# Performance work log

Measured on AMD Instinct MI355X. Metric: run time of the kernel, lower is better.

The kernel has to match this reference:

```python
import jax, jax.numpy as jnp
import numpy as np

N = 4096
IN_F = 128
OUT_F = 64
H = 4
NEG_SLOPE = 0.2


def setup_inputs() -> dict:
    key = jax.random.key(0)
    kx, ka, kw, kadj = jax.random.split(key, 4)
    x = jax.random.normal(kx, (N, IN_F), dtype=jnp.float32)
    adj = (jax.random.uniform(kadj, (N, N)) < 0.01).astype(jnp.float32)
    # xavier-uniform-ish params
    W = jax.random.uniform(kw, (IN_F, OUT_F * H), dtype=jnp.float32,
                           minval=-1.0, maxval=1.0) * float(np.sqrt(6.0 / (IN_F + OUT_F * H)))
    a = jax.random.uniform(ka, (H, 2 * OUT_F), dtype=jnp.float32,
                           minval=-1.0, maxval=1.0) * float(np.sqrt(6.0 / (H + 2 * OUT_F)))
    return {"x": x, "adj": adj, "W": W, "a": a}


def reference(x, adj, W, a):
    n = x.shape[0]
    h = (x @ W).reshape(n, H, OUT_F)                      # [N,H,F]
    a_src = a[:, :OUT_F]                                  # [H,F]
    a_tgt = a[:, OUT_F:]                                  # [H,F]
    attn_src = jnp.einsum('nhf,hf->nh', h, a_src)         # [N,H]
    attn_tgt = jnp.einsum('nhf,hf->nh', h, a_tgt)         # [N,H]
    # e[i,h,j] = attn_src[i,h] + attn_tgt[j,h]
    e = attn_src[:, :, None] + attn_tgt.T[None, :, :]     # [N,H,N]
    e = jnp.where(e > 0, e, NEG_SLOPE * e)                # leaky_relu(0.2)
    adj_self = adj + jnp.eye(n, dtype=adj.dtype)
    mask = (adj_self != 0)[:, None, :]                    # [N,1,N]
    e = jnp.where(mask, e, -jnp.inf)
    attention = jax.nn.softmax(e, axis=-1)                # [N,H,N]
    attention = jnp.nan_to_num(attention, nan=0.0)
    # dropout is identity at eval time
    out = jnp.einsum('nhj,jhf->nhf', attention, h)        # [N,H,F]
    return out.reshape(n, H * OUT_F)
```

## Files before the change

kernel.cpp:

```cpp
#include <hip/hip_runtime.h>
#include <hip/hip_bf16.h>

#define N_NODES 4096
#define IN_FEAT 128
#define OUT_FEAT 64
#define NHEAD 4
#define HID 256
#define NEG_SLOPE 0.2f
#define MAXC 256
#define GEMM_BLOCKS 256
#define SCAN_BLOCKS 1024

typedef float f4 __attribute__((ext_vector_type(4)));

__global__ __launch_bounds__(256) void k_prep(
    const float* __restrict__ x, const float* __restrict__ adj,
    const float* __restrict__ W, const float* __restrict__ a,
    float* __restrict__ h, float* __restrict__ attn_src,
    float* __restrict__ attn_tgt,
    unsigned short* __restrict__ nbrs, int* __restrict__ deg)
{
    __shared__ f4 xs4[64][32];
    __shared__ float red_s[4][64];
    __shared__ float red_t[4][64];

    const int t = threadIdx.x;
    const int lane = t & 63;
    const int wv = t >> 6;

    if (blockIdx.x < GEMM_BLOCKS) {
        const int rb = blockIdx.x >> 2;
        const int cb = blockIdx.x & 3;
        const int row0 = rb * 64;
        const int tc4 = (t >> 4) * 4;
        const int c0 = cb * 64 + tc4;
        const int tr = t & 15;

        {
            const f4* xg = reinterpret_cast<const f4*>(x) + (size_t)row0 * 32;
            const int kq = t & 31;
            #pragma unroll
            for (int it = 0; it < 8; ++it) {
                const int r = it * 8 + (t >> 5);
                xs4[r][kq ^ ((r >> 2) & 7)] = xg[r * 32 + kq];
            }
        }
        __syncthreads();

        f4 acc[4] = {};

        for (int kq = 0; kq < 32; ++kq) {
            f4 wvv[4];
            #pragma unroll
            for (int kk = 0; kk < 4; ++kk)
                wvv[kk] = *reinterpret_cast<const f4*>(W + (kq * 4 + kk) * HID + c0);
            f4 xv[4];
            #pragma unroll
            for (int j = 0; j < 4; ++j)
                xv[j] = xs4[tr * 4 + j][kq ^ (tr & 7)];
            #pragma unroll
            for (int kk = 0; kk < 4; ++kk)
                #pragma unroll
                for (int j = 0; j < 4; ++j)
                    acc[j] += xv[j][kk] * wvv[kk];
        }

        #pragma unroll
        for (int j = 0; j < 4; ++j) {
            const int row = row0 + tr * 4 + j;
            *reinterpret_cast<f4*>(h + (size_t)row * HID + c0) = acc[j];
        }

        const f4 asv = *reinterpret_cast<const f4*>(a + cb * 2 * OUT_FEAT + tc4);
        const f4 atv = *reinterpret_cast<const f4*>(a + cb * 2 * OUT_FEAT + OUT_FEAT + tc4);
        #pragma unroll
        for (int j = 0; j < 4; ++j) {
            float s = acc[j][0] * asv[0] + acc[j][1] * asv[1]
                    + acc[j][2] * asv[2] + acc[j][3] * asv[3];
            float g = acc[j][0] * atv[0] + acc[j][1] * atv[1]
                    + acc[j][2] * atv[2] + acc[j][3] * atv[3];
            s += __shfl_xor(s, 16, 64); s += __shfl_xor(s, 32, 64);
            g += __shfl_xor(g, 16, 64); g += __shfl_xor(g, 32, 64);
            if (((t >> 4) & 3) == 0) {
                red_s[wv][tr * 4 + j] = s;
                red_t[wv][tr * 4 + j] = g;
            }
        }
        __syncthreads();
        if (t < 64) {
            const float s = red_s[0][t] + red_s[1][t] + red_s[2][t] + red_s[3][t];
            const float g = red_t[0][t] + red_t[1][t] + red_t[2][t] + red_t[3][t];
            attn_src[(row0 + t) * NHEAD + cb] = s;
            attn_tgt[(row0 + t) * NHEAD + cb] = g;
        }
    } else {
        const int i = (blockIdx.x - GEMM_BLOCKS) * 4 + wv;

        const float4* arow = reinterpret_cast<const float4*>(adj + (size_t)i * N_NODES);
        float4 v[16];
        #pragma unroll
        for (int u = 0; u < 16; ++u) v[u] = arow[u * 64 + lane];

        unsigned long long m = 0ull;
        #pragma unroll
        for (int u = 0; u < 16; ++u) {
            const int jb = u * 256 + lane * 4;
            if (v[u].x != 0.f || (jb + 0) == i) m |= 1ull << (u * 4 + 0);
            if (v[u].y != 0.f || (jb + 1) == i) m |= 1ull << (u * 4 + 1);
            if (v[u].z != 0.f || (jb + 2) == i) m |= 1ull << (u * 4 + 2);
            if (v[u].w != 0.f || (jb + 3) == i) m |= 1ull << (u * 4 + 3);
        }
        const int cnt = __popcll(m);

        int incl = cnt;
        #pragma unroll
        for (int d = 1; d < 64; d <<= 1) {
            int u2 = __shfl_up(incl, d, 64);
            if (lane >= d) incl += u2;
        }
        int off = incl - cnt;
        if (lane == 63) deg[i] = (incl < MAXC) ? incl : MAXC;

        unsigned short* nl = nbrs + (size_t)i * MAXC;
        unsigned long long mm = m;
        while (mm) {
            const int b = __ffsll((unsigned long long)mm) - 1;
            mm &= mm - 1;
            const int j = ((b >> 2) * 256) + lane * 4 + (b & 3);
            if (off < MAXC) nl[off] = (unsigned short)j;
            ++off;
        }
    }
}

__global__ __launch_bounds__(256) void k_agg(
    const unsigned short* __restrict__ nbrs, const int* __restrict__ deg,
    const float* __restrict__ h, const float* __restrict__ attn_src,
    const float* __restrict__ attn_tgt, float* __restrict__ out)
{
    __shared__ float p[NHEAD][MAXC];
    __shared__ unsigned short nl[MAXC];

    const int i = blockIdx.x;
    const int t = threadIdx.x;
    const int lane = t & 63;
    const int head = t >> 6;

    const int d = deg[i];
    nl[t] = (t < d) ? nbrs[(size_t)i * MAXC + t] : (unsigned short)0;
    __syncthreads();

    const float srcv = attn_src[i * NHEAD + head];
    const int rnd = (d + 3) & ~3;
    float lmax = -1e30f;
    for (int idx = lane; idx < rnd; idx += 64) {
        if (idx < d) {
            float e = srcv + attn_tgt[nl[idx] * NHEAD + head];
            e = (e > 0.f) ? e : NEG_SLOPE * e;
            p[head][idx] = e;
            lmax = fmaxf(lmax, e);
        } else {
            p[head][idx] = 0.f;
        }
    }
    #pragma unroll
    for (int s = 32; s; s >>= 1) lmax = fmaxf(lmax, __shfl_xor(lmax, s, 64));
    float ssum = 0.f;
    for (int idx = lane; idx < d; idx += 64) {
        float pe = __expf(p[head][idx] - lmax);
        p[head][idx] = pe;
        ssum += pe;
    }
    #pragma unroll
    for (int s = 32; s; s >>= 1) ssum += __shfl_xor(ssum, s, 64);
    const float inv = 1.0f / ssum;

    const int g  = lane >> 4;
    const int f4i = lane & 15;
    const float* hbase = h + head * OUT_FEAT + f4i * 4;
    float4 acc = {0.f, 0.f, 0.f, 0.f};
    for (int idx4 = 0; idx4 < d; idx4 += 4) {
        const int j   = nl[idx4 + g];
        const float pw = p[head][idx4 + g];
        const float4 hv = *reinterpret_cast<const float4*>(hbase + (size_t)j * HID);
        acc.x += pw * hv.x; acc.y += pw * hv.y;
        acc.z += pw * hv.z; acc.w += pw * hv.w;
    }
    #pragma unroll
    for (int s = 16; s <= 32; s <<= 1) {
        acc.x += __shfl_xor(acc.x, s, 64);
        acc.y += __shfl_xor(acc.y, s, 64);
        acc.z += __shfl_xor(acc.z, s, 64);
        acc.w += __shfl_xor(acc.w, s, 64);
    }
    if (g == 0) {
        float4 o = {acc.x * inv, acc.y * inv, acc.z * inv, acc.w * inv};
        *reinterpret_cast<float4*>(out + (size_t)i * HID + head * OUT_FEAT + f4i * 4) = o;
    }
}

extern "C" void kernel_launch(void* const* d_in, const int* in_sizes, int n_in,
                              void* d_out, int out_size, void* d_ws, size_t ws_size,
                              hipStream_t stream)
{
    const float* x   = (const float*)d_in[0];
    const float* adj = (const float*)d_in[1];
    const float* W   = (const float*)d_in[2];
    const float* a   = (const float*)d_in[3];
    float* out = (float*)d_out;

    char* ws = (char*)d_ws;
    float* h         = (float*)ws;
    float* attn_src  = (float*)(ws + (size_t)N_NODES * HID * 4);
    float* attn_tgt  = attn_src + (size_t)N_NODES * NHEAD;
    unsigned short* nbrs = (unsigned short*)(attn_tgt + (size_t)N_NODES * NHEAD);
    int* deg         = (int*)(nbrs + (size_t)N_NODES * MAXC);

    k_prep<<<GEMM_BLOCKS + SCAN_BLOCKS, 256, 0, stream>>>(
        x, adj, W, a, h, attn_src, attn_tgt, nbrs, deg);
    k_agg<<<N_NODES, 256, 0, stream>>>(nbrs, deg, h, attn_src, attn_tgt, out);
}
```

Before: 37.39 us.

## Split fused prep kernel into separate adjacency scan and GEMM kernels

The combined prep kernel, which branched by block index between the x@W GEMM and the adjacency scan, is split into two kernels launched back to back on the same stream. The scan now uses nontemporal loads for the 64 MB adjacency stream. This removes divergent register and LDS allocation across the two roles, so the scan blocks no longer reserve the GEMM's shared memory. The cost is an extra launch and the loss of concurrency between GEMM and scan within one grid.

Result: slower. 48.13 us (+28.7%).

```diff
diff --git a/kernel.cpp b/kernel.cpp
--- a/kernel.cpp
+++ b/kernel.cpp
@@ -9,127 +9,128 @@
 #define NEG_SLOPE 0.2f
 #define MAXC 256
 #define GEMM_BLOCKS 256
-#define SCAN_BLOCKS 1024
 
 typedef float f4 __attribute__((ext_vector_type(4)));
 
-__global__ __launch_bounds__(256) void k_prep(
-    const float* __restrict__ x, const float* __restrict__ adj,
-    const float* __restrict__ W, const float* __restrict__ a,
-    float* __restrict__ h, float* __restrict__ attn_src,
-    float* __restrict__ attn_tgt,
+__global__ __launch_bounds__(256) void k_scan(
+    const float* __restrict__ adj,
     unsigned short* __restrict__ nbrs, int* __restrict__ deg)
+{
+    const int t = threadIdx.x;
+    const int lane = t & 63;
+    const int wv = t >> 6;
+    const int i = blockIdx.x * 4 + wv;
+
+    const f4* arow = reinterpret_cast<const f4*>(adj + (size_t)i * N_NODES);
+    f4 v[16];
+    #pragma unroll
+    for (int u = 0; u < 16; ++u)
+        v[u] = __builtin_nontemporal_load(&arow[u * 64 + lane]);
+
+    unsigned long long m = 0ull;
+    #pragma unroll
+    for (int u = 0; u < 16; ++u) {
+        const int jb = u * 256 + lane * 4;
+        if (v[u][0] != 0.f || (jb + 0) == i) m |= 1ull << (u * 4 + 0);
+        if (v[u][1] != 0.f || (jb + 1) == i) m |= 1ull << (u * 4 + 1);
+        if (v[u][2] != 0.f || (jb + 2) == i) m |= 1ull << (u * 4 + 2);
+        if (v[u][3] != 0.f || (jb + 3) == i) m |= 1ull << (u * 4 + 3);
+    }
+    const int cnt = __popcll(m);
+
+    int incl = cnt;
+    #pragma unroll
+    for (int d = 1; d < 64; d <<= 1) {
+        int u2 = __shfl_up(incl, d, 64);
+        if (lane >= d) incl += u2;
+    }
+    int off = incl - cnt;
+    if (lane == 63) deg[i] = (incl < MAXC) ? incl : MAXC;
+
+    unsigned short* nl = nbrs + (size_t)i * MAXC;
+    unsigned long long mm = m;
+    while (mm) {
+        const int b = __ffsll(mm) - 1;
+        mm &= mm - 1;
+        const int j = ((b >> 2) * 256) + lane * 4 + (b & 3);
+        if (off < MAXC) nl[off] = (unsigned short)j;
+        ++off;
+    }
+}
+
+__global__ __launch_bounds__(256) void k_gemm(
+    const float* __restrict__ x, const float* __restrict__ W,
+    const float* __restrict__ a, float* __restrict__ h,
+    float* __restrict__ attn_src, float* __restrict__ attn_tgt)
 {
     __shared__ f4 xs4[64][32];
     __shared__ float red_s[4][64];
     __shared__ float red_t[4][64];
 
     const int t = threadIdx.x;
-    const int lane = t & 63;
+    const int rb = blockIdx.x >> 2;
+    const int cb = blockIdx.x & 3;
+    const int row0 = rb * 64;
+    const int tc4 = (t >> 4) * 4;
+    const int c0 = cb * 64 + tc4;
+    const int tr = t & 15;
     const int wv = t >> 6;
 
-    if (blockIdx.x < GEMM_BLOCKS) {
-        const int rb = blockIdx.x >> 2;
-        const int cb = blockIdx.x & 3;
-        const int row0 = rb * 64;
-        const int tc4 = (t >> 4) * 4;
-        const int c0 = cb * 64 + tc4;
-        const int tr = t & 15;
-
-        {
-            const f4* xg = reinterpret_cast<const f4*>(x) + (size_t)row0 * 32;
-            const int kq = t & 31;
-            #pragma unroll
-            for (int it = 0; it < 8; ++it) {
-                const int r = it * 8 + (t >> 5);
-                xs4[r][kq ^ ((r >> 2) & 7)] = xg[r * 32 + kq];
-            }
+    {
+        const f4* xg = reinterpret_cast<const f4*>(x) + (size_t)row0 * 32;
+        const int kq = t & 31;
+        #pragma unroll
+        for (int it = 0; it < 8; ++it) {
+            const int r = it * 8 + (t >> 5);
+            xs4[r][kq ^ ((r >> 2) & 7)] = xg[r * 32 + kq];
         }
-        __syncthreads();
-
-        f4 acc[4] = {};
-
-        for (int kq = 0; kq < 32; ++kq) {
-            f4 wvv[4];
-            #pragma unroll
-            for (int kk = 0; kk < 4; ++kk)
-                wvv[kk] = *reinterpret_cast<const f4*>(W + (kq * 4 + kk) * HID + c0);
-            f4 xv[4];
+    }
+    __syncthreads();
+
+    f4 acc[4] = {};
+    for (int kq = 0; kq < 32; ++kq) {
+        f4 wvv[4];
+        #pragma unroll
+        for (int kk = 0; kk < 4; ++kk)
+            wvv[kk] = *reinterpret_cast<const f4*>(W + (kq * 4 + kk) * HID + c0);
+        f4 xv[4];
+        #pragma unroll
+        for (int j = 0; j < 4; ++j)
+            xv[j] = xs4[tr * 4 + j][kq ^ (tr & 7)];
+        #pragma unroll
+        for (int kk = 0; kk < 4; ++kk)
             #pragma unroll
             for (int j = 0; j < 4; ++j)
-                xv[j] = xs4[tr * 4 + j][kq ^ (tr & 7)];
-            #pragma unroll
-            for (int kk = 0; kk < 4; ++kk)
-                #pragma unroll
-                for (int j = 0; j < 4; ++j)
-                    acc[j] += xv[j][kk] * wvv[kk];
+                acc[j] += xv[j][kk] * wvv[kk];
+    }
+
+    #pragma unroll
+    for (int j = 0; j < 4; ++j) {
+        const int row = row0 + tr * 4 + j;
+        *reinterpret_cast<f4*>(h + (size_t)row * HID + c0) = acc[j];
+    }
+
+    const f4 asv = *reinterpret_cast<const f4*>(a + cb * 2 * OUT_FEAT + tc4);
+    const f4 atv = *reinterpret_cast<const f4*>(a + cb * 2 * OUT_FEAT + OUT_FEAT + tc4);
+    #pragma unroll
+    for (int j = 0; j < 4; ++j) {
+        float s = acc[j][0] * asv[0] + acc[j][1] * asv[1]
+                + acc[j][2] * asv[2] + acc[j][3] * asv[3];
+        float g = acc[j][0] * atv[0] + acc[j][1] * atv[1]
+                + acc[j][2] * atv[2] + acc[j][3] * atv[3];
+        s += __shfl_xor(s, 16, 64); s += __shfl_xor(s, 32, 64);
+        g += __shfl_xor(g, 16, 64); g += __shfl_xor(g, 32, 64);
+        if (((t >> 4) & 3) == 0) {
+            red_s[wv][tr * 4 + j] = s;
+            red_t[wv][tr * 4 + j] = g;
         }
-
-        #pragma unroll
-        for (int j = 0; j < 4; ++j) {
-            const int row = row0 + tr * 4 + j;
-            *reinterpret_cast<f4*>(h + (size_t)row * HID + c0) = acc[j];
-        }
-
-        const f4 asv = *reinterpret_cast<const f4*>(a + cb * 2 * OUT_FEAT + tc4);
-        const f4 atv = *reinterpret_cast<const f4*>(a + cb * 2 * OUT_FEAT + OUT_FEAT + tc4);
-        #pragma unroll
-        for (int j = 0; j < 4; ++j) {
-            float s = acc[j][0] * asv[0] + acc[j][1] * asv[1]
-                    + acc[j][2] * asv[2] + acc[j][3] * asv[3];
-            float g = acc[j][0] * atv[0] + acc[j][1] * atv[1]
-                    + acc[j][2] * atv[2] + acc[j][3] * atv[3];
-            s += __shfl_xor(s, 16, 64); s += __shfl_xor(s, 32, 64);
-            g += __shfl_xor(g, 16, 64); g += __shfl_xor(g, 32, 64);
-            if (((t >> 4) & 3) == 0) {
-                red_s[wv][tr * 4 + j] = s;
-                red_t[wv][tr * 4 + j] = g;
-            }
-        }
-        __syncthreads();
-        if (t < 64) {
-            const float s = red_s[0][t] + red_s[1][t] + red_s[2][t] + red_s[3][t];
-            const float g = red_t[0][t] + red_t[1][t] + red_t[2][t] + red_t[3][t];
-            attn_src[(row0 + t) * NHEAD + cb] = s;
-            attn_tgt[(row0 + t) * NHEAD + cb] = g;
-        }
-    } else {
-        const int i = (blockIdx.x - GEMM_BLOCKS) * 4 + wv;
-
-        const float4* arow = reinterpret_cast<const float4*>(adj + (size_t)i * N_NODES);
-        float4 v[16];
-        #pragma unroll
-        for (int u = 0; u < 16; ++u) v[u] = arow[u * 64 + lane];
-
-        unsigned long long m = 0ull;
-        #pragma unroll
-        for (int u = 0; u < 16; ++u) {
-            const int jb = u * 256 + lane * 4;
-            if (v[u].x != 0.f || (jb + 0) == i) m |= 1ull << (u * 4 + 0);
-            if (v[u].y != 0.f || (jb + 1) == i) m |= 1ull << (u * 4 + 1);
-            if (v[u].z != 0.f || (jb + 2) == i) m |= 1ull << (u * 4 + 2);
-            if (v[u].w != 0.f || (jb + 3) == i) m |= 1ull << (u * 4 + 3);
-        }
-        const int cnt = __popcll(m);
-
-        int incl = cnt;
-        #pragma unroll
-        for (int d = 1; d < 64; d <<= 1) {
-            int u2 = __shfl_up(incl, d, 64);
-            if (lane >= d) incl += u2;
-        }
-        int off = incl - cnt;
-        if (lane == 63) deg[i] = (incl < MAXC) ? incl : MAXC;
-
-        unsigned short* nl = nbrs + (size_t)i * MAXC;
-        unsigned long long mm = m;
-        while (mm) {
-            const int b = __ffsll((unsigned long long)mm) - 1;
-            mm &= mm - 1;
-            const int j = ((b >> 2) * 256) + lane * 4 + (b & 3);
-            if (off < MAXC) nl[off] = (unsigned short)j;
-            ++off;
-        }
+    }
+    __syncthreads();
+    if (t < 64) {
+        const float s = red_s[0][t] + red_s[1][t] + red_s[2][t] + red_s[3][t];
+        const float g = red_t[0][t] + red_t[1][t] + red_t[2][t] + red_t[3][t];
+        attn_src[(row0 + t) * NHEAD + cb] = s;
+        attn_tgt[(row0 + t) * NHEAD + cb] = g;
     }
 }
 
@@ -216,7 +217,7 @@
     unsigned short* nbrs = (unsigned short*)(attn_tgt + (size_t)N_NODES * NHEAD);
     int* deg         = (int*)(nbrs + (size_t)N_NODES * MAXC);
 
-    k_prep<<<GEMM_BLOCKS + SCAN_BLOCKS, 256, 0, stream>>>(
-        x, adj, W, a, h, attn_src, attn_tgt, nbrs, deg);
+    k_scan<<<N_NODES / 4, 256, 0, stream>>>(adj, nbrs, deg);
+    k_gemm<<<GEMM_BLOCKS, 256, 0, stream>>>(x, W, a, h, attn_src, attn_tgt);
     k_agg<<<N_NODES, 256, 0, stream>>>(nbrs, deg, h, attn_src, attn_tgt, out);
 }
```

## Stream adjacency into nibble bitmap, build neighbor lists inside aggregation kernel

Applied to the files above, without the earlier changes.

The adjacency scan in the prep kernel no longer builds per-row neighbor lists with wave scans. It becomes a flat grid-strided stream that turns each float4 of the 64MB adjacency into a 4-bit nibble byte, with coalesced reads and byte writes. The aggregation kernel then reads its row's 1KB bitmap, packs the nibbles into 64-bit masks, adds the self-loop, and compacts neighbor indices in shared memory. The aim is to make the dominant adjacency read purely bandwidth-bound and drop the nbrs/deg round trip, at the cost of extra per-block setup work in the aggregation kernel.

New measurement: 38.54 us. 3.1% more time.

```diff
diff --git a/kernel.cpp b/kernel.cpp
--- a/kernel.cpp
+++ b/kernel.cpp
@@ -1,5 +1,4 @@
 #include <hip/hip_runtime.h>
-#include <hip/hip_bf16.h>
 
 #define N_NODES 4096
 #define IN_FEAT 128
@@ -9,7 +8,10 @@
 #define NEG_SLOPE 0.2f
 #define MAXC 256
 #define GEMM_BLOCKS 256
-#define SCAN_BLOCKS 1024
+#define STREAM_BLOCKS 512
+#define STREAM_THREADS (STREAM_BLOCKS * 256)
+#define TOT_F4 (N_NODES * (N_NODES / 4))
+#define OUTER (TOT_F4 / STREAM_THREADS / 8)
 
 typedef float f4 __attribute__((ext_vector_type(4)));
 
@@ -17,16 +19,13 @@
     const float* __restrict__ x, const float* __restrict__ adj,
     const float* __restrict__ W, const float* __restrict__ a,
     float* __restrict__ h, float* __restrict__ attn_src,
-    float* __restrict__ attn_tgt,
-    unsigned short* __restrict__ nbrs, int* __restrict__ deg)
+    float* __restrict__ attn_tgt, unsigned char* __restrict__ bitmap)
 {
     __shared__ f4 xs4[64][32];
     __shared__ float red_s[4][64];
     __shared__ float red_t[4][64];
 
     const int t = threadIdx.x;
-    const int lane = t & 63;
-    const int wv = t >> 6;
 
     if (blockIdx.x < GEMM_BLOCKS) {
         const int rb = blockIdx.x >> 2;
@@ -35,6 +34,7 @@
         const int tc4 = (t >> 4) * 4;
         const int c0 = cb * 64 + tc4;
         const int tr = t & 15;
+        const int wv = t >> 6;
 
         {
             const f4* xg = reinterpret_cast<const f4*>(x) + (size_t)row0 * 32;
@@ -48,7 +48,6 @@
         __syncthreads();
 
         f4 acc[4] = {};
-
         for (int kq = 0; kq < 32; ++kq) {
             f4 wvv[4];
             #pragma unroll
@@ -94,61 +93,75 @@
             attn_tgt[(row0 + t) * NHEAD + cb] = g;
         }
     } else {
-        const int i = (blockIdx.x - GEMM_BLOCKS) * 4 + wv;
-
-        const float4* arow = reinterpret_cast<const float4*>(adj + (size_t)i * N_NODES);
-        float4 v[16];
-        #pragma unroll
-        for (int u = 0; u < 16; ++u) v[u] = arow[u * 64 + lane];
-
-        unsigned long long m = 0ull;
-        #pragma unroll
-        for (int u = 0; u < 16; ++u) {
-            const int jb = u * 256 + lane * 4;
-            if (v[u].x != 0.f || (jb + 0) == i) m |= 1ull << (u * 4 + 0);
-            if (v[u].y != 0.f || (jb + 1) == i) m |= 1ull << (u * 4 + 1);
-            if (v[u].z != 0.f || (jb + 2) == i) m |= 1ull << (u * 4 + 2);
-            if (v[u].w != 0.f || (jb + 3) == i) m |= 1ull << (u * 4 + 3);
-        }
-        const int cnt = __popcll(m);
-
-        int incl = cnt;
-        #pragma unroll
-        for (int d = 1; d < 64; d <<= 1) {
-            int u2 = __shfl_up(incl, d, 64);
-            if (lane >= d) incl += u2;
-        }
-        int off = incl - cnt;
-        if (lane == 63) deg[i] = (incl < MAXC) ? incl : MAXC;
-
-        unsigned short* nl = nbrs + (size_t)i * MAXC;
-        unsigned long long mm = m;
-        while (mm) {
-            const int b = __ffsll((unsigned long long)mm) - 1;
-            mm &= mm - 1;
-            const int j = ((b >> 2) * 256) + lane * 4 + (b & 3);
-            if (off < MAXC) nl[off] = (unsigned short)j;
-            ++off;
+        const int g = (blockIdx.x - GEMM_BLOCKS) * 256 + t;
+        const f4* src = reinterpret_cast<const f4*>(adj);
+        for (int r = 0; r < OUTER; ++r) {
+            f4 v[8];
+            #pragma unroll
+            for (int u = 0; u < 8; ++u)
+                v[u] = src[(size_t)(r * 8 + u) * STREAM_THREADS + g];
+            #pragma unroll
+            for (int u = 0; u < 8; ++u) {
+                const unsigned nib = (v[u][0] != 0.f ? 1u : 0u)
+                                   | (v[u][1] != 0.f ? 2u : 0u)
+                                   | (v[u][2] != 0.f ? 4u : 0u)
+                                   | (v[u][3] != 0.f ? 8u : 0u);
+                bitmap[(size_t)(r * 8 + u) * STREAM_THREADS + g] = (unsigned char)nib;
+            }
         }
     }
 }
 
 __global__ __launch_bounds__(256) void k_agg(
-    const unsigned short* __restrict__ nbrs, const int* __restrict__ deg,
-    const float* __restrict__ h, const float* __restrict__ attn_src,
-    const float* __restrict__ attn_tgt, float* __restrict__ out)
+    const unsigned char* __restrict__ bitmap, const float* __restrict__ h,
+    const float* __restrict__ attn_src, const float* __restrict__ attn_tgt,
+    float* __restrict__ out)
 {
     __shared__ float p[NHEAD][MAXC];
     __shared__ unsigned short nl[MAXC];
+    __shared__ int sdeg;
 
     const int i = blockIdx.x;
     const int t = threadIdx.x;
     const int lane = t & 63;
     const int head = t >> 6;
 
-    const int d = deg[i];
-    nl[t] = (t < d) ? nbrs[(size_t)i * MAXC + t] : (unsigned short)0;
+    if (t < 64) {
+        for (int k = lane; k < MAXC; k += 64) nl[k] = 0;
+
+        const unsigned long long* wrow = reinterpret_cast<const unsigned long long*>(
+            bitmap + (size_t)i * (N_NODES / 4));
+        unsigned long long w0 = wrow[lane * 2 + 0];
+        unsigned long long w1 = wrow[lane * 2 + 1];
+
+        #define PACK(b) ({ unsigned long long _b = (b) & 0x0F0F0F0F0F0F0F0Full; \
+            _b = (_b | (_b >> 4))  & 0x00FF00FF00FF00FFull;                      \
+            _b = (_b | (_b >> 8))  & 0x0000FFFF0000FFFFull;                      \
+            _b = (_b | (_b >> 16)) & 0x00000000FFFFFFFFull; _b; })
+        unsigned long long m = PACK(w0) | (PACK(w1) << 32);
+        #undef PACK
+        if ((i >> 6) == lane) m |= 1ull << (i & 63);
+
+        const int cnt = __popcll(m);
+        int incl = cnt;
+        #pragma unroll
+        for (int d2 = 1; d2 < 64; d2 <<= 1) {
+            int u2 = __shfl_up(incl, d2, 64);
+            if (lane >= d2) incl += u2;
+        }
+        int off = incl - cnt;
+        int total = __shfl(incl, 63, 64);
+        if (total > MAXC) total = MAXC;
+        if (lane == 0) sdeg = total;
+        while (m) {
+            const int b = __ffsll(m) - 1;
+            m &= m - 1;
+            if (off < MAXC) nl[off] = (unsigned short)(lane * 64 + b);
+            ++off;
+        }
+    }
     __syncthreads();
+    const int d = sdeg;
 
     const float srcv = attn_src[i * NHEAD + head];
     const int rnd = (d + 3) & ~3;
@@ -213,10 +226,9 @@
     float* h         = (float*)ws;
     float* attn_src  = (float*)(ws + (size_t)N_NODES * HID * 4);
     float* attn_tgt  = attn_src + (size_t)N_NODES * NHEAD;
-    unsigned short* nbrs = (unsigned short*)(attn_tgt + (size_t)N_NODES * NHEAD);
-    int* deg         = (int*)(nbrs + (size_t)N_NODES * MAXC);
-
-    k_prep<<<GEMM_BLOCKS + SCAN_BLOCKS, 256, 0, stream>>>(
-        x, adj, W, a, h, attn_src, attn_tgt, nbrs, deg);
-    k_agg<<<N_NODES, 256, 0, stream>>>(nbrs, deg, h, attn_src, attn_tgt, out);
+    unsigned char* bitmap = (unsigned char*)(attn_tgt + (size_t)N_NODES * NHEAD);
+
+    k_prep<<<GEMM_BLOCKS + STREAM_BLOCKS, 256, 0, stream>>>(
+        x, adj, W, a, h, attn_src, attn_tgt, bitmap);
+    k_agg<<<N_NODES, 256, 0, stream>>>(bitmap, h, attn_src, attn_tgt, out);
 }
```
